# Kernel tuning notes

Measured on AMD Instinct MI355X. Metric: run time of the kernel, lower is better.

The kernel has to match this reference:

```python
import jax, jax.numpy as jnp
import numpy as np

SAMPLE_RATE = 16000
M = 10          # welch averaging window (frames)
R = 30          # long-term window (frames)
EPS = 1e-5
WIN_LEN = 25    # source bug: ms value used as window length in samples


def _hamming_sq_sum(n):
    # torch.hamming_window(n, periodic=True): 0.54 - 0.46*cos(2*pi*k/n)
    k = np.arange(n)
    w = 0.54 - 0.46 * np.cos(2.0 * np.pi * k / n)
    return np.float32((w ** 2).sum())


def _windowed_mean(x, w):
    """y[:, i, :] = mean(x[:, max(0, i-w):i, :]) for i>=1, y[:,0,:]=0.
    Vectorized via prefix sums: replaces the per-frame Python loop."""
    B, T, F = x.shape
    c = jnp.cumsum(x, axis=1)
    c = jnp.concatenate([jnp.zeros((B, 1, F), x.dtype), c], axis=1)  # c[:, i] = sum of first i frames
    idx = jnp.arange(T)
    lo = jnp.maximum(idx - w, 0)
    cnt = jnp.minimum(idx, w).astype(x.dtype)            # window length per frame (0 at i=0)
    mean = (c[:, idx] - c[:, lo]) / jnp.maximum(cnt, 1)[None, :, None]
    return mean  # mean[:,0,:] == 0 since numerator is 0 there


def setup_inputs() -> dict:
    key = jax.random.key(0)
    x = jax.random.normal(key, (32, 3000, 201, 2), dtype=jnp.float32)
    return {"x": x}


def reference(x) -> jnp.ndarray:
    B, T, F, _ = x.shape
    # speechbrain spectral_magnitude (power=1): power spectrum re^2 + im^2
    spectr = jnp.sum(x * x, axis=-1) / M                         # (B, T, F)
    # welch scaling: /fs * sum(window^2), interior bins doubled
    scale = jnp.ones((F,), x.dtype).at[1:-1].set(2.0)
    s = spectr * (_hamming_sq_sum(WIN_LEN) / SAMPLE_RATE) * scale[None, None, :]
    welch = _windowed_mean(s, M)                                 # (B, T, F)
    # long-term geometric and arithmetic means over R frames of the welch spectrum
    t0 = (jnp.arange(T) == 0)[None, :, None]
    geo = jnp.exp(_windowed_mean(jnp.log(welch + EPS), R)) - EPS
    gm = jnp.where(t0, 0.0, geo) + EPS                           # frame 0 forced to 0 (as in source)
    am = _windowed_mean(welch, R) + EPS
    flatness = -jnp.sum(jnp.log10(gm / am), axis=-1, keepdims=True)  # (B, T, 1)
    return flatness
```

## Files before the change

kernel.cpp:

```cpp
#include <hip/hip_runtime.h>


constexpr int TT = 3000;
constexpr int FF = 201;
constexpr int BB = 32;
constexpr int W1 = 10;
constexpr int W2 = 30;
constexpr int HALO = 40;
constexpr int LTILE = 60;
constexpr int NT = 50;
#define EPSV 1e-5f
#define CSCALE (9.935f / 160000.0f)
#define LOG10_2 0.3010299956639812f

#define SUPERGROUP(DYN, TERM)                                                  \
  {                                                                            \
    _Pragma("unroll") for (int g = 0; g < 6; ++g) {                            \
      float2* cb = (g & 1) ? b1 : b0;          \
      float2* nb = (g & 1) ? b0 : b1;                                          \
      const float2* pn = ((TERM) && g == 5) ? pf : (pf + 5 * FF);              \
      _Pragma("unroll") for (int j = 0; j < 5; ++j) nb[j] = pn[j * FF];        \
      float rr[5];                                                             \
      _Pragma("unroll") for (int j = 0; j < 5; ++j) {                          \
        const int fr = g * 5 + j;        \
        const int t = t0 + m0 + fr;                                            \
        float inv10, inv30;                                                    \
        if (DYN) {                                                             \
          inv10 = 1.0f / (float)max(min(t, W1), 1);                            \
          inv30 = 1.0f / (float)max(min(t, W2), 1);                            \
        } else {                                                               \
          inv10 = 0.1f;                                                        \
          inv30 = (1.0f / 30.0f);                                              \
        }                                                                      \
        float welch = ssum * inv10;                                            \
        float lw = __log2f(welch + EPSV);                                      \
        float am = fmaf(wsum, inv30, EPSV);                                    \
        float la = __log2f(am);                                                \
        rr[j] = (la - lsum * inv30) * LOG10_2;                                 \
        float wold = w_ring[fr];                                               \
        if (DYN) lsum += lw;                   \
        else     lsum += lw - __log2f(wold + EPSV);    \
        wsum += welch - wold;                                                  \
        w_ring[fr] = welch;                                                    \
        float sv = fmaf(cb[j].x, cb[j].x, cb[j].y * cb[j].y) * cs;             \
        ssum += sv - s_ring[fr % 10];                                          \
        s_ring[fr % 10] = sv;                                                  \
      }                                                                        \
        \
      _Pragma("unroll") for (int off = 16; off >= 2; off >>= 1) {              \
        _Pragma("unroll") for (int j = 0; j < 5; ++j)                          \
            rr[j] += __shfl_xor(rr[j], off, 64);                               \
      }                                                                        \
      if ((lane & 30) == 0) {                                                  \
        const int p = (lane & 1) | ((lane >> 4) & 2);                          \
        _Pragma("unroll") for (int j = 0; j < 5; ++j)                          \
            ((float*)&part[wv][m0 + g * 5 + j])[p] = rr[j];                    \
      }                                                                        \
      pf = pn;                                                                 \
    }                                                                          \
    m0 += 30;                                                                  \
  }

__global__ __launch_bounds__(256, 2)
void ltsf_kernel(const float2* __restrict__ x, float* __restrict__ out) {
  const int tid = threadIdx.x;
  const int tile = blockIdx.x;
  const int b = blockIdx.y;
  const int t0 = tile * LTILE;
  const bool first = (tile == 0);
  const int tstart = first ? 0 : (t0 - HALO);
  const int lane = tid & 63;
  const int wv = tid >> 6;

  const int f = (tid < FF) ? tid : (FF - 1);
  float cs = (tid < FF) ? ((tid == 0 || tid == FF - 1) ? 1.0f : 2.0f) : 0.0f;
  cs *= CSCALE;

  const float2* xb = x + (size_t)b * TT * FF;

  __shared__ float4 part[4][LTILE];

  float s_ring[W1], w_ring[W2];
#pragma unroll
  for (int j = 0; j < W1; ++j) s_ring[j] = 0.f;
#pragma unroll
  for (int j = 0; j < W2; ++j) w_ring[j] = 0.f;
  float ssum = 0.f, wsum = 0.f, lsum = 0.f;

  float2 b0[5], b1[5];
  const float2* pf = xb + (size_t)tstart * FF + f;

#pragma unroll
  for (int j = 0; j < 5; ++j) b0[j] = pf[j * FF];

  int m0 = 0;

  if (!first) {
#pragma unroll
    for (int g = 0; g < 2; ++g) {
      float2* cb = (g & 1) ? b1 : b0;
      float2* nb = (g & 1) ? b0 : b1;
      const float2* pn = pf + 5 * FF;
#pragma unroll
      for (int j = 0; j < 5; ++j) nb[j] = pn[j * FF];
#pragma unroll
      for (int j = 0; j < 5; ++j) {
        float sv = fmaf(cb[j].x, cb[j].x, cb[j].y * cb[j].y) * cs;
        ssum += sv;
        s_ring[g * 5 + j] = sv;
      }
      pf = pn;
    }
#pragma unroll
    for (int g = 0; g < 6; ++g) {
      float2* cb = (g & 1) ? b1 : b0;
      float2* nb = (g & 1) ? b0 : b1;
      const float2* pn = pf + 5 * FF;
#pragma unroll
      for (int j = 0; j < 5; ++j) nb[j] = pn[j * FF];
#pragma unroll
      for (int j = 0; j < 5; ++j) {
        const int fr = g * 5 + j;
        float welch = ssum * 0.1f;
        float lw = __log2f(welch + EPSV);
        wsum += welch; w_ring[fr] = welch;
        lsum += lw;
        float sv = fmaf(cb[j].x, cb[j].x, cb[j].y * cb[j].y) * cs;
        ssum += sv - s_ring[fr % 10];
        s_ring[fr % 10] = sv;
      }
      pf = pn;
    }
  }

  if (first) {
    SUPERGROUP(true, false);
    SUPERGROUP(false, true);
  } else {
    SUPERGROUP(false, false);
    SUPERGROUP(false, true);
  }

  __syncthreads();
  if (tid < LTILE) {
    float4 v0 = part[0][tid], v1 = part[1][tid];
    float4 v2 = part[2][tid], v3 = part[3][tid];
    float v = ((v0.x + v0.y) + (v0.z + v0.w)) + ((v1.x + v1.y) + (v1.z + v1.w)) +
              ((v2.x + v2.y) + (v2.z + v2.w)) + ((v3.x + v3.y) + (v3.z + v3.w));
    if (first && tid == 0) v = 0.f;
    out[(size_t)b * TT + t0 + tid] = v;
  }
}

extern "C" void kernel_launch(void* const* d_in, const int* in_sizes, int n_in,
                              void* d_out, int out_size, void* d_ws, size_t ws_size,
                              hipStream_t stream) {
  const float2* x = (const float2*)d_in[0];
  float* out = (float*)d_out;
  dim3 grid(NT, BB);
  ltsf_kernel<<<grid, 256, 0, stream>>>(x, out);
}
```

Baseline: 225.6 us.

## Triple-buffer frame prefetch two groups ahead and swap grid axes

Replaces the double-buffered register prefetch with a three-buffer rotation, so each group of five frames is loaded two groups before it is consumed. The warmup and main loops become fully unrolled per-group macros. The grid is also transposed so blockIdx.x indexes the batch and blockIdx.y the time tile, which changes the block dispatch order and so the memory locality. The deeper prefetch is meant to hide global load latency in the serial recurrence, at the cost of more registers under the 256-thread, 2-block launch bounds.

```diff
diff --git a/kernel.cpp b/kernel.cpp
--- a/kernel.cpp
+++ b/kernel.cpp
@@ -13,59 +13,91 @@
 #define CSCALE (9.935f / 160000.0f)
 #define LOG10_2 0.3010299956639812f
 
-#define SUPERGROUP(DYN, TERM)                                                  \
+#define BUFSEL(I) ((I) % 3 == 0 ? bufA : ((I) % 3 == 1 ? bufB : bufC))
+
+#define PF_GROUP(GI, GTOT)                                                     \
   {                                                                            \
-    _Pragma("unroll") for (int g = 0; g < 6; ++g) {                            \
-      float2* cb = (g & 1) ? b1 : b0;          \
-      float2* nb = (g & 1) ? b0 : b1;                                          \
-      const float2* pn = ((TERM) && g == 5) ? pf : (pf + 5 * FF);              \
-      _Pragma("unroll") for (int j = 0; j < 5; ++j) nb[j] = pn[j * FF];        \
-      float rr[5];                                                             \
-      _Pragma("unroll") for (int j = 0; j < 5; ++j) {                          \
-        const int fr = g * 5 + j;        \
-        const int t = t0 + m0 + fr;                                            \
-        float inv10, inv30;                                                    \
-        if (DYN) {                                                             \
-          inv10 = 1.0f / (float)max(min(t, W1), 1);                            \
-          inv30 = 1.0f / (float)max(min(t, W2), 1);                            \
-        } else {                                                               \
-          inv10 = 0.1f;                                                        \
-          inv30 = (1.0f / 30.0f);                                              \
-        }                                                                      \
-        float welch = ssum * inv10;                                            \
-        float lw = __log2f(welch + EPSV);                                      \
-        float am = fmaf(wsum, inv30, EPSV);                                    \
-        float la = __log2f(am);                                                \
-        rr[j] = (la - lsum * inv30) * LOG10_2;                                 \
-        float wold = w_ring[fr];                                               \
-        if (DYN) lsum += lw;                   \
-        else     lsum += lw - __log2f(wold + EPSV);    \
-        wsum += welch - wold;                                                  \
-        w_ring[fr] = welch;                                                    \
-        float sv = fmaf(cb[j].x, cb[j].x, cb[j].y * cb[j].y) * cs;             \
-        ssum += sv - s_ring[fr % 10];                                          \
-        s_ring[fr % 10] = sv;                                                  \
+    const float2* pn = ((GI) + 2 < (GTOT)) ? (pf2 + 5 * FF) : pf2;             \
+    float2* nb = BUFSEL((GI) + 2);                                             \
+    _Pragma("unroll") for (int j = 0; j < 5; ++j) nb[j] = pn[j * FF];          \
+    pf2 = pn;                                                                  \
+  }
+
+#define WARMA_GROUP(GI)                                                        \
+  {                                                                            \
+    PF_GROUP(GI, 20);                                                          \
+    float2* cb = BUFSEL(GI);                                                   \
+    _Pragma("unroll") for (int j = 0; j < 5; ++j) {                            \
+      float sv = fmaf(cb[j].x, cb[j].x, cb[j].y * cb[j].y) * cs;               \
+      ssum += sv;                                                              \
+      s_ring[(GI) * 5 + j] = sv;                                               \
+    }                                                                          \
+  }
+
+#define WARMB_GROUP(GI)                                                        \
+  {                                                                            \
+    PF_GROUP(GI, 20);                                                          \
+    float2* cb = BUFSEL(GI);                                                   \
+    _Pragma("unroll") for (int j = 0; j < 5; ++j) {                            \
+      const int fr = ((GI) - 2) * 5 + j;                                       \
+      float welch = ssum * 0.1f;                                               \
+      float lw = __log2f(welch + EPSV);                                        \
+      wsum += welch; w_ring[fr] = welch;                                       \
+      lsum += lw;                                                              \
+      float sv = fmaf(cb[j].x, cb[j].x, cb[j].y * cb[j].y) * cs;               \
+      ssum += sv - s_ring[fr % 10];                                            \
+      s_ring[fr % 10] = sv;                                                    \
+    }                                                                          \
+  }
+
+#define MAIN_GROUP(GI, GBASE, GTOT, DYN)                                       \
+  {                                                                            \
+    PF_GROUP(GI, GTOT);                                                        \
+    float2* cb = BUFSEL(GI);                                                   \
+    float rr[5];                                                               \
+    _Pragma("unroll") for (int j = 0; j < 5; ++j) {                            \
+      const int m = ((GI) - (GBASE)) * 5 + j;                                  \
+      const int fr = m % 30;                                                   \
+      const int t = t0 + m;                                                    \
+      float inv10, inv30;                                                      \
+      if (DYN) {                                                               \
+        inv10 = 1.0f / (float)max(min(t, W1), 1);                              \
+        inv30 = 1.0f / (float)max(min(t, W2), 1);                              \
+      } else {                                                                 \
+        inv10 = 0.1f;                                                          \
+        inv30 = (1.0f / 30.0f);                                                \
       }                                                                        \
+      float welch = ssum * inv10;                                              \
+      float lw = __log2f(welch + EPSV);                                        \
+      float am = fmaf(wsum, inv30, EPSV);                                      \
+      float la = __log2f(am);                                                  \
+      rr[j] = (la - lsum * inv30) * LOG10_2;                                   \
+      float wold = w_ring[fr];                                                 \
+      if (DYN) lsum += lw;                                                     \
+      else     lsum += lw - __log2f(wold + EPSV);                              \
+      wsum += welch - wold;                                                    \
+      w_ring[fr] = welch;                                                      \
+      float sv = fmaf(cb[j].x, cb[j].x, cb[j].y * cb[j].y) * cs;               \
+      ssum += sv - s_ring[fr % 10];                                            \
+      s_ring[fr % 10] = sv;                                                    \
+    }                                                                          \
         \
-      _Pragma("unroll") for (int off = 16; off >= 2; off >>= 1) {              \
-        _Pragma("unroll") for (int j = 0; j < 5; ++j)                          \
-            rr[j] += __shfl_xor(rr[j], off, 64);                               \
-      }                                                                        \
-      if ((lane & 30) == 0) {                                                  \
-        const int p = (lane & 1) | ((lane >> 4) & 2);                          \
-        _Pragma("unroll") for (int j = 0; j < 5; ++j)                          \
-            ((float*)&part[wv][m0 + g * 5 + j])[p] = rr[j];                    \
-      }                                                                        \
-      pf = pn;                                                                 \
+    _Pragma("unroll") for (int off = 16; off >= 2; off >>= 1) {                \
+      _Pragma("unroll") for (int j = 0; j < 5; ++j)                            \
+          rr[j] += __shfl_xor(rr[j], off, 64);                                 \
     }                                                                          \
-    m0 += 30;                                                                  \
+    if ((lane & 30) == 0) {                                                    \
+      const int p = (lane & 1) | ((lane >> 4) & 2);                            \
+      _Pragma("unroll") for (int j = 0; j < 5; ++j)                            \
+          ((float*)&part[wv][((GI) - (GBASE)) * 5 + j])[p] = rr[j];            \
+    }                                                                          \
   }
 
 __global__ __launch_bounds__(256, 2)
 void ltsf_kernel(const float2* __restrict__ x, float* __restrict__ out) {
   const int tid = threadIdx.x;
-  const int tile = blockIdx.x;
-  const int b = blockIdx.y;
+  const int b = blockIdx.x;
+  const int tile = blockIdx.y;
   const int t0 = tile * LTILE;
   const bool first = (tile == 0);
   const int tstart = first ? 0 : (t0 - HALO);
@@ -87,58 +119,32 @@
   for (int j = 0; j < W2; ++j) w_ring[j] = 0.f;
   float ssum = 0.f, wsum = 0.f, lsum = 0.f;
 
-  float2 b0[5], b1[5];
-  const float2* pf = xb + (size_t)tstart * FF + f;
+  float2 bufA[5], bufB[5], bufC[5];
 
+  const float2* p0 = xb + (size_t)tstart * FF + f;
 #pragma unroll
-  for (int j = 0; j < 5; ++j) b0[j] = pf[j * FF];
-
-  int m0 = 0;
+  for (int j = 0; j < 5; ++j) bufA[j] = p0[j * FF];
+  const float2* pf2 = p0 + 5 * FF;
+#pragma unroll
+  for (int j = 0; j < 5; ++j) bufB[j] = pf2[j * FF];
 
   if (!first) {
-#pragma unroll
-    for (int g = 0; g < 2; ++g) {
-      float2* cb = (g & 1) ? b1 : b0;
-      float2* nb = (g & 1) ? b0 : b1;
-      const float2* pn = pf + 5 * FF;
-#pragma unroll
-      for (int j = 0; j < 5; ++j) nb[j] = pn[j * FF];
-#pragma unroll
-      for (int j = 0; j < 5; ++j) {
-        float sv = fmaf(cb[j].x, cb[j].x, cb[j].y * cb[j].y) * cs;
-        ssum += sv;
-        s_ring[g * 5 + j] = sv;
-      }
-      pf = pn;
-    }
-#pragma unroll
-    for (int g = 0; g < 6; ++g) {
-      float2* cb = (g & 1) ? b1 : b0;
-      float2* nb = (g & 1) ? b0 : b1;
-      const float2* pn = pf + 5 * FF;
-#pragma unroll
-      for (int j = 0; j < 5; ++j) nb[j] = pn[j * FF];
-#pragma unroll
-      for (int j = 0; j < 5; ++j) {
-        const int fr = g * 5 + j;
-        float welch = ssum * 0.1f;
-        float lw = __log2f(welch + EPSV);
-        wsum += welch; w_ring[fr] = welch;
-        lsum += lw;
-        float sv = fmaf(cb[j].x, cb[j].x, cb[j].y * cb[j].y) * cs;
-        ssum += sv - s_ring[fr % 10];
-        s_ring[fr % 10] = sv;
-      }
-      pf = pn;
-    }
-  }
-
-  if (first) {
-    SUPERGROUP(true, false);
-    SUPERGROUP(false, true);
+    WARMA_GROUP(0)  WARMA_GROUP(1)
+    WARMB_GROUP(2)  WARMB_GROUP(3)  WARMB_GROUP(4)
+    WARMB_GROUP(5)  WARMB_GROUP(6)  WARMB_GROUP(7)
+    MAIN_GROUP(8,  8, 20, false)  MAIN_GROUP(9,  8, 20, false)
+    MAIN_GROUP(10, 8, 20, false)  MAIN_GROUP(11, 8, 20, false)
+    MAIN_GROUP(12, 8, 20, false)  MAIN_GROUP(13, 8, 20, false)
+    MAIN_GROUP(14, 8, 20, false)  MAIN_GROUP(15, 8, 20, false)
+    MAIN_GROUP(16, 8, 20, false)  MAIN_GROUP(17, 8, 20, false)
+    MAIN_GROUP(18, 8, 20, false)  MAIN_GROUP(19, 8, 20, false)
   } else {
-    SUPERGROUP(false, false);
-    SUPERGROUP(false, true);
+    MAIN_GROUP(0,  0, 12, true)   MAIN_GROUP(1,  0, 12, true)
+    MAIN_GROUP(2,  0, 12, true)   MAIN_GROUP(3,  0, 12, true)
+    MAIN_GROUP(4,  0, 12, true)   MAIN_GROUP(5,  0, 12, true)
+    MAIN_GROUP(6,  0, 12, false)  MAIN_GROUP(7,  0, 12, false)
+    MAIN_GROUP(8,  0, 12, false)  MAIN_GROUP(9,  0, 12, false)
+    MAIN_GROUP(10, 0, 12, false)  MAIN_GROUP(11, 0, 12, false)
   }
 
   __syncthreads();
@@ -157,6 +163,6 @@
                               hipStream_t stream) {
   const float2* x = (const float2*)d_in[0];
   float* out = (float*)d_out;
-  dim3 grid(NT, BB);
+  dim3 grid(BB, NT);
   ltsf_kernel<<<grid, 256, 0, stream>>>(x, out);
 }
```

After: 223.1 us. No clear change (-1.1%).
